# Kernel tuning notes

Hardware: AMD Instinct MI355X
Metric: run time of the kernel (lower is better)

## Reference

```python
import jax, jax.numpy as jnp
import numpy as np

EPS = 1e-3  # Keras BatchNormalization default epsilon
HEADS = 4
KEY_DEPTH = 16   # k
INTRA = 1        # u
VAL_DEPTH = 64   # v = kernel_out // heads = 256 // 4
C_IN = 256
B, HH, WW = 16, 32, 32
N = HH * WW      # == size of positional embedding


def setup_inputs() -> dict:
    key = jax.random.key(0)
    ks = jax.random.split(key, 6)
    x = jax.random.normal(ks[0], (B, HH, WW, C_IN), dtype=jnp.float32)
    # 1x1 conv kernels == dense matrices over the channel dim
    Wq = jax.random.normal(ks[1], (C_IN, KEY_DEPTH * HEADS), dtype=jnp.float32) * 0.05
    Wk = jax.random.normal(ks[2], (C_IN, KEY_DEPTH * INTRA), dtype=jnp.float32) * 0.05
    Wv = jax.random.normal(ks[3], (C_IN, VAL_DEPTH * INTRA), dtype=jnp.float32) * 0.05
    # BatchNorm (inference mode) parameters
    gamma_q = jnp.ones((KEY_DEPTH * HEADS,), jnp.float32)
    beta_q = jnp.zeros((KEY_DEPTH * HEADS,), jnp.float32)
    mean_q = jnp.zeros((KEY_DEPTH * HEADS,), jnp.float32)
    var_q = jnp.ones((KEY_DEPTH * HEADS,), jnp.float32)
    gamma_v = jnp.ones((VAL_DEPTH * INTRA,), jnp.float32)
    beta_v = jnp.zeros((VAL_DEPTH * INTRA,), jnp.float32)
    mean_v = jnp.zeros((VAL_DEPTH * INTRA,), jnp.float32)
    var_v = jnp.ones((VAL_DEPTH * INTRA,), jnp.float32)
    # Positional embedding: [size, size, key_depth, intra_depth], uniform init
    E = jax.random.uniform(ks[4], (N, N, KEY_DEPTH, INTRA), dtype=jnp.float32)
    return {
        'x': x, 'Wq': Wq, 'Wk': Wk, 'Wv': Wv,
        'gamma_q': gamma_q, 'beta_q': beta_q, 'mean_q': mean_q, 'var_q': var_q,
        'gamma_v': gamma_v, 'beta_v': beta_v, 'mean_v': mean_v, 'var_v': var_v,
        'E': E,
    }


def _bn(t, gamma, beta, mean, var):
    return gamma * (t - mean) / jnp.sqrt(var + EPS) + beta


def reference(x, Wq, Wk, Wv, gamma_q, beta_q, mean_q, var_q,
              gamma_v, beta_v, mean_v, var_v, E):
    b, hh, ww, _ = x.shape
    n = hh * ww
    # 1x1 conv projections (context c == x)
    q = jnp.einsum('bhwc,cd->bhwd', x, Wq)           # [b,hh,ww,h*k]
    k = jnp.einsum('bhwc,cd->bhwd', x, Wk)           # [b,hh,ww,u*k]
    v = jnp.einsum('bhwc,cd->bhwd', x, Wv)           # [b,hh,ww,u*v]
    q = _bn(q, gamma_q, beta_q, mean_q, var_q)
    v = _bn(v, gamma_v, beta_v, mean_v, var_v)
    # softmax over the channel axis (faithful to the source code)
    k = jax.nn.softmax(k, axis=-1)
    # rearranges: b hh ww (h k) -> b h k n ; b hh ww (u k) -> b u k n ; b hh ww (u v) -> b u v n
    q = q.reshape(b, n, HEADS, KEY_DEPTH).transpose(0, 2, 3, 1)   # [b,h,k,n]
    k = k.reshape(b, n, INTRA, KEY_DEPTH).transpose(0, 2, 3, 1)   # [b,u,k,n]
    v = v.reshape(b, n, INTRA, VAL_DEPTH).transpose(0, 2, 3, 1)   # [b,u,v,n]
    # content lambda: sum over intra-depth and positions
    lam_c = jnp.einsum('bukn,buvn->bkv', k, v)                    # [b,k,v]
    Yc = jnp.einsum('bhkn,bkv->bhvn', q, lam_c)                   # [b,h,v,n]
    # positional lambdas: E[n,m,k,u] contracted with v[b,u,v,m]
    lam_p = jnp.einsum('nmku,buvm->bnkv', E, v)                   # [b,n,k,v]
    Yp = jnp.einsum('bhkn,bnkv->bhvn', q, lam_p)                  # [b,h,v,n]
    Y = Yc + Yp                                                    # [b,h,v,n]
    # b h v n -> b hh ww (h v)
    out = Y.transpose(0, 3, 1, 2).reshape(b, hh, ww, HEADS * VAL_DEPTH)
    return out
```

## Files before the change

### kernel.cpp

```cpp
#include <hip/hip_runtime.h>
#include <stdint.h>

#define EPS 1e-3f

typedef __bf16 bf16x8 __attribute__((ext_vector_type(8)));
typedef float  f32x4  __attribute__((ext_vector_type(4)));

static __device__ __forceinline__ uint16_t f2bf(float f) {
  union { float f; uint32_t u; } v; v.f = f;
  uint32_t u = v.u;
  uint32_t r = u + 0x7fffu + ((u >> 16) & 1u);
  return (uint16_t)(r >> 16);
}
static __device__ __forceinline__ uint32_t pack2bf(float lo, float hi) {
  union { uint16_t h[2]; uint32_t u; } r;
  r.h[0] = f2bf(lo); r.h[1] = f2bf(hi);
  return r.u;
}
static __device__ __forceinline__ void gload_lds16(const void* g, void* l) {
  __builtin_amdgcn_global_load_lds(
      (const __attribute__((address_space(1))) unsigned int*)g,
      (__attribute__((address_space(3))) unsigned int*)l, 16, 0, 0);
}

__global__ __launch_bounds__(256) void wprep(
    const float* __restrict__ Wq, const float* __restrict__ Wk,
    const float* __restrict__ Wv, uint16_t* __restrict__ WtP)
{
  const int col = blockIdx.x, t = threadIdx.x;
  float val = (col < 64) ? Wq[t * 64 + col]
            : (col < 80) ? Wk[t * 16 + (col - 64)]
                         : Wv[t * 64 + (col - 80)];
  WtP[col * 264 + t] = f2bf(val);
}

__global__ __launch_bounds__(256) void proj_mfma(
    const float* __restrict__ x, const uint16_t* __restrict__ WtP,
    const float* __restrict__ gq, const float* __restrict__ bq,
    const float* __restrict__ mq, const float* __restrict__ vq,
    const float* __restrict__ gv, const float* __restrict__ bv,
    const float* __restrict__ mv, const float* __restrict__ vvp,
    float* __restrict__ Qf, uint16_t* __restrict__ VbfT,
    float* __restrict__ part)
{
  __shared__ __align__(16) char smem[111616];
  uint16_t* const xA = (uint16_t*)smem;
  char* const Wt = smem + 33792;

  const int t = threadIdx.x;
  const int wid = t >> 6, lane = t & 63;
  const int bid = blockIdx.x;
  const int b = bid >> 4, mc = bid & 15;
  const int r0 = b * 1024 + mc * 64;

#pragma unroll
  for (int i = 0; i < 19; ++i) {
    int off = (i * 256 + t) * 16;
    gload_lds16((const char*)WtP + off, Wt + off);
  }
  {
    const int row = t >> 2, ks0 = (t & 3) * 64;
    const float* src = x + (size_t)(r0 + row) * 256 + ks0;
    uint16_t* dstp = xA + row * 264 + ks0;
#pragma unroll
    for (int i = 0; i < 8; ++i) {
      float4 d0 = *(const float4*)(src + i * 8);
      float4 d1 = *(const float4*)(src + i * 8 + 4);
      union { uint16_t u[8]; uint4 q; } pk;
      pk.u[0] = f2bf(d0.x); pk.u[1] = f2bf(d0.y);
      pk.u[2] = f2bf(d0.z); pk.u[3] = f2bf(d0.w);
      pk.u[4] = f2bf(d1.x); pk.u[5] = f2bf(d1.y);
      pk.u[6] = f2bf(d1.z); pk.u[7] = f2bf(d1.w);
      *(uint4*)(dstp + i * 8) = pk.q;
    }
  }
  __syncthreads();

  f32x4 acc[9];
#pragma unroll
  for (int f = 0; f < 9; ++f) acc[f] = f32x4{0.f, 0.f, 0.f, 0.f};
  const int arow = wid * 16 + (lane & 15);
#pragma unroll
  for (int kst = 0; kst < 8; ++kst) {
    const int sb = kst * 64 + ((lane >> 4) << 4);
    bf16x8 af = *(const bf16x8*)((const char*)xA + arow * 528 + sb);
#pragma unroll
    for (int f = 0; f < 9; ++f) {
      const int crow = f * 16 + (lane & 15);
      bf16x8 bfr = *(const bf16x8*)(Wt + crow * 528 + sb);
      acc[f] = __builtin_amdgcn_mfma_f32_16x16x32_bf16(af, bfr, acc[f], 0, 0, 0);
    }
  }

  const int cl = lane & 15;
  const int rbase = wid * 16 + ((lane >> 4) << 2);

  float qs[4], qb[4], qm[4], vs[4], vb[4], vm[4];
#pragma unroll
  for (int f = 0; f < 4; ++f) {
    const int c = f * 16 + cl;
    qs[f] = gq[c] * rsqrtf(vq[c] + EPS); qb[f] = bq[c]; qm[f] = mq[c];
    vs[f] = gv[c] * rsqrtf(vvp[c] + EPS); vb[f] = bv[c]; vm[f] = mv[c];
  }
#pragma unroll
  for (int f = 0; f < 4; ++f)
#pragma unroll
    for (int r = 0; r < 4; ++r)
      Qf[(size_t)(r0 + rbase + r) * 64 + f * 16 + cl] =
          (acc[f][r] - qm[f]) * qs[f] + qb[f];
  float ex[4];
#pragma unroll
  for (int r = 0; r < 4; ++r) {
    float kv = acc[4][r];
    float mx = kv;
#pragma unroll
    for (int d = 1; d < 16; d <<= 1) mx = fmaxf(mx, __shfl_xor(mx, d, 64));
    float e = __expf(kv - mx);
    float sm = e;
#pragma unroll
    for (int d = 1; d < 16; d <<= 1) sm += __shfl_xor(sm, d, 64);
    ex[r] = e / sm;
  }
  float vv[4][4];
#pragma unroll
  for (int f = 0; f < 4; ++f)
#pragma unroll
    for (int r = 0; r < 4; ++r)
      vv[f][r] = (acc[5 + f][r] - vm[f]) * vs[f] + vb[f];

  __syncthreads();
  float* const vt = (float*)smem;
  float* const ks = (float*)(smem + 64 * 65 * 4);
#pragma unroll
  for (int r = 0; r < 4; ++r) ks[(rbase + r) * 20 + cl] = ex[r];
#pragma unroll
  for (int f = 0; f < 4; ++f)
#pragma unroll
    for (int r = 0; r < 4; ++r) vt[(rbase + r) * 65 + f * 16 + cl] = vv[f][r];
  __syncthreads();

  {
    const int v = t & 63, grp = t >> 6;
#pragma unroll
    for (int h = 0; h < 2; ++h) {
      union { uint16_t u16[8]; uint4 q; } pk;
#pragma unroll
      for (int i = 0; i < 8; ++i)
        pk.u16[i] = f2bf(vt[(grp * 16 + h * 8 + i) * 65 + v]);
      *(uint4*)&VbfT[(size_t)(b * 64 + v) * 1024 + mc * 64 + grp * 16 + h * 8] = pk.q;
    }
  }
  {
    const int kq = t >> 6, v = t & 63;
    float a0 = 0.f, a1 = 0.f, a2 = 0.f, a3 = 0.f;
#pragma unroll 4
    for (int m = 0; m < 64; ++m) {
      float vvx = vt[m * 65 + v];
      a0 = fmaf(ks[m * 20 + kq * 4 + 0], vvx, a0);
      a1 = fmaf(ks[m * 20 + kq * 4 + 1], vvx, a1);
      a2 = fmaf(ks[m * 20 + kq * 4 + 2], vvx, a2);
      a3 = fmaf(ks[m * 20 + kq * 4 + 3], vvx, a3);
    }
    float* dst = part + ((size_t)(b * 16 + mc) << 10) + (kq * 4) * 64 + v;
    dst[0] = a0; dst[64] = a1; dst[128] = a2; dst[192] = a3;
  }
}

__global__ __launch_bounds__(256) void lamc_reduce(const float* __restrict__ part,
                                                   float* __restrict__ Lc)
{
  const int gid = blockIdx.x * 256 + threadIdx.x;
  const int b = gid >> 10, r = gid & 1023;
  const float* p = part + ((size_t)b << 14) + r;
  float s = 0.f;
#pragma unroll
  for (int mc = 0; mc < 16; ++mc) s += p[mc << 10];
  Lc[((size_t)b << 10) + r] = s;
}

__global__ __launch_bounds__(512, 2) void gemm_out(
    const float* __restrict__ E,
    const uint16_t* __restrict__ VbfT,
    const float* __restrict__ Qf,
    const float* __restrict__ Lc,
    float* __restrict__ out)
{
  __shared__ __align__(16) char smem[131072];
  char* const A0 = smem;
  char* const B0 = smem + 32768;
  char* const A1 = smem + 65536;
  char* const B1 = smem + 98304;

  const int t = threadIdx.x;
  const int wid = t >> 6, lane = t & 63;
  const int wm = wid >> 2, wn = wid & 3;
  const int bid = blockIdx.x;
  const int xcd = bid & 7, idx = bid >> 3;
  const int rb = xcd * 8 + (idx >> 2);
  const int cb = idx & 3;
  const int col0 = cb * 256;
  const int n0 = rb * 16;

  const int kq = t & 3;
  const int mp = (t >> 2) & 31;
  const int nb = t >> 7;
  const float* Eb = E + ((size_t)n0 << 14);

  int awoff[4][4];
#pragma unroll
  for (int it = 0; it < 4; ++it)
#pragma unroll
    for (int j = 0; j < 4; ++j) {
      int row = (it * 4 + nb) * 16 + kq * 4 + j;
      awoff[it][j] = row * 128 + ((mp * 4) ^ ((row & 7) << 4));
    }

  const uint16_t* bptr[4];
  int bdst[4];
  {
    const uint16_t* Bb = VbfT + ((size_t)col0 << 10);
#pragma unroll
    for (int it = 0; it < 4; ++it) {
      int id = it * 512 + t;
      int row = id >> 3, seg = id & 7;
      bptr[it] = Bb + (row << 10) + ((seg ^ (row & 7)) << 3);
      bdst[it] = id * 16;
    }
  }

  f32x4 acc[8][4];
#pragma unroll
  for (int i = 0; i < 8; ++i)
#pragma unroll
    for (int j = 0; j < 4; ++j) acc[i][j] = f32x4{0.f, 0.f, 0.f, 0.f};

  float4 ra[4], rbx[4];

#pragma unroll
  for (int it = 0; it < 4; ++it) {
    size_t base = ((size_t)(it * 4 + nb) << 14) + ((size_t)(mp * 2) << 4) + (kq << 2);
    ra[it]  = *(const float4*)(Eb + base);
    rbx[it] = *(const float4*)(Eb + base + 16);
  }
#pragma unroll
  for (int it = 0; it < 4; ++it) gload_lds16(bptr[it], B0 + bdst[it]);
#pragma unroll
  for (int it = 0; it < 4; ++it) {
    const float* da = (const float*)&ra[it];
    const float* db = (const float*)&rbx[it];
#pragma unroll
    for (int j = 0; j < 4; ++j)
      *(uint32_t*)(A0 + awoff[it][j]) = pack2bf(da[j], db[j]);
  }
  __syncthreads();

#pragma unroll 1
  for (int kt = 0; kt < 16; ++kt) {
    char* Ac = (kt & 1) ? A1 : A0;
    char* Bc = (kt & 1) ? B1 : B0;
    char* An = (kt & 1) ? A0 : A1;
    char* Bn = (kt & 1) ? B0 : B1;
    if (kt < 15) {
      const int m0n = (kt + 1) * 64;
#pragma unroll
      for (int it = 0; it < 4; ++it) {
        size_t base = ((size_t)(it * 4 + nb) << 14) +
                      ((size_t)(m0n + mp * 2) << 4) + (kq << 2);
        ra[it]  = *(const float4*)(Eb + base);
        rbx[it] = *(const float4*)(Eb + base + 16);
      }
#pragma unroll
      for (int it = 0; it < 4; ++it) gload_lds16(bptr[it] + m0n, Bn + bdst[it]);
    }
    __builtin_amdgcn_s_setprio(1);
#pragma unroll
    for (int kk = 0; kk < 2; ++kk) {
      bf16x8 a[8], b[4];
      const int s = kk * 4 + (lane >> 4);
#pragma unroll
      for (int i = 0; i < 8; ++i) {
        int row = wm * 128 + i * 16 + (lane & 15);
        a[i] = *(const bf16x8*)(Ac + row * 128 + ((s ^ (row & 7)) << 4));
      }
#pragma unroll
      for (int j = 0; j < 4; ++j) {
        int row = wn * 64 + j * 16 + (lane & 15);
        b[j] = *(const bf16x8*)(Bc + row * 128 + ((s ^ (row & 7)) << 4));
      }
#pragma unroll
      for (int i = 0; i < 8; ++i)
#pragma unroll
        for (int j = 0; j < 4; ++j)
          acc[i][j] = __builtin_amdgcn_mfma_f32_16x16x32_bf16(a[i], b[j], acc[i][j], 0, 0, 0);
    }
    __builtin_amdgcn_s_setprio(0);
    if (kt < 15) {
#pragma unroll
      for (int it = 0; it < 4; ++it) {
        const float* da = (const float*)&ra[it];
        const float* db = (const float*)&rbx[it];
#pragma unroll
        for (int j = 0; j < 4; ++j)
          *(uint32_t*)(An + awoff[it][j]) = pack2bf(da[j], db[j]);
      }
    }
    __syncthreads();
  }

  float* Cs = (float*)smem;
  const int b0 = cb * 4;
#pragma unroll
  for (int p = 0; p < 4; ++p) {
    if (wm == (p >> 1)) {
#pragma unroll
      for (int il = 0; il < 4; ++il) {
        const int i = ((p & 1) << 2) + il;
#pragma unroll
        for (int j = 0; j < 4; ++j) {
          const int col = wn * 64 + j * 16 + (lane & 15);
          const int bb = b0 + (col >> 6), v = col & 63;
#pragma unroll
          for (int r = 0; r < 4; ++r) {
            const int rl = il * 16 + ((lane >> 4) << 2) + r;
            const int k = rl & 15;
            Cs[rl * 258 + col] = acc[i][j][r] + Lc[(size_t)(((bb << 4) + k) << 6) + v];
          }
        }
      }
    }
    __syncthreads();
    {
      const int v = t & 63;
#pragma unroll
      for (int c = 0; c < 8; ++c) {
        const int combo = (wid << 3) + c;
        const int n_l = combo >> 4;
        const int b_l = (combo >> 2) & 3;
        const int h = combo & 3;
        const int n = n0 + (p << 2) + n_l;
        const int bb = b0 + b_l;
        const float* qp = Qf + (((size_t)(bb << 10) + n) << 6) + (h << 4);
        float sum = 0.f;
#pragma unroll
        for (int k = 0; k < 16; ++k)
          sum = fmaf(qp[k], Cs[((n_l << 4) + k) * 258 + (b_l << 6) + v], sum);
        out[(((size_t)(bb << 10) + n) << 8) + (h << 6) + v] = sum;
      }
    }
    __syncthreads();
  }
}

extern "C" void kernel_launch(void* const* d_in, const int* in_sizes, int n_in,
                              void* d_out, int out_size, void* d_ws, size_t ws_size,
                              hipStream_t stream) {
  const float* x   = (const float*)d_in[0];
  const float* Wq  = (const float*)d_in[1];
  const float* Wk  = (const float*)d_in[2];
  const float* Wv  = (const float*)d_in[3];
  const float* gq  = (const float*)d_in[4];
  const float* bq  = (const float*)d_in[5];
  const float* mq  = (const float*)d_in[6];
  const float* vq  = (const float*)d_in[7];
  const float* gv  = (const float*)d_in[8];
  const float* bv  = (const float*)d_in[9];
  const float* mv  = (const float*)d_in[10];
  const float* vvp = (const float*)d_in[11];
  const float* E   = (const float*)d_in[12];
  float* out = (float*)d_out;

  char* ws = (char*)d_ws;
  uint16_t* VbfT = (uint16_t*)(ws);
  float*    Qf   = (float*)(ws + (size_t)(2 << 20));
  float*    part = (float*)(ws + (size_t)(6 << 20));
  float*    Lc   = (float*)(ws + (size_t)(7 << 20));
  uint16_t* WtP  = (uint16_t*)(ws + (size_t)(7 << 20) + 65536);

  hipLaunchKernelGGL(wprep, dim3(144), dim3(256), 0, stream, Wq, Wk, Wv, WtP);
  hipLaunchKernelGGL(proj_mfma, dim3(256), dim3(256), 0, stream, x, WtP,
                     gq, bq, mq, vq, gv, bv, mv, vvp, Qf, VbfT, part);
  hipLaunchKernelGGL(lamc_reduce, dim3(64), dim3(256), 0, stream, part, Lc);
  hipLaunchKernelGGL(gemm_out, dim3(256), dim3(512), 0, stream, E, VbfT, Qf, Lc, out);
}
```

Baseline: 75.38 us.

## Double proj_mfma block size to 128 rows and use native bf16 conversion

The projection kernel now runs 128 blocks of 512 threads, each handling 128 rows instead of 64, so the weight tile loaded into LDS is amortised over twice as many rows. The partial lambda_c reduction is split into two halves per block so the part buffer layout stays the same. Manual round-to-nearest-even bf16 packing is replaced with the compiler's native __bf16 conversion, which may map to hardware convert instructions. The risks are fewer blocks than CUs and a larger LDS footprint (about 140 KB) per block.

```diff
diff --git a/kernel.cpp b/kernel.cpp
--- a/kernel.cpp
+++ b/kernel.cpp
@@ -7,14 +7,11 @@
 typedef float  f32x4  __attribute__((ext_vector_type(4)));
 
 static __device__ __forceinline__ uint16_t f2bf(float f) {
-  union { float f; uint32_t u; } v; v.f = f;
-  uint32_t u = v.u;
-  uint32_t r = u + 0x7fffu + ((u >> 16) & 1u);
-  return (uint16_t)(r >> 16);
-}
-static __device__ __forceinline__ uint32_t pack2bf(float lo, float hi) {
-  union { uint16_t h[2]; uint32_t u; } r;
-  r.h[0] = f2bf(lo); r.h[1] = f2bf(hi);
+  union { __bf16 b; uint16_t u; } r; r.b = (__bf16)f; return r.u;
+}
+static __device__ __forceinline__ uint32_t cvt2(float lo, float hi) {
+  union { __bf16 b[2]; uint32_t u; } r;
+  r.b[0] = (__bf16)lo; r.b[1] = (__bf16)hi;
   return r.u;
 }
 static __device__ __forceinline__ void gload_lds16(const void* g, void* l) {
@@ -34,7 +31,7 @@
   WtP[col * 264 + t] = f2bf(val);
 }
 
-__global__ __launch_bounds__(256) void proj_mfma(
+__global__ __launch_bounds__(512) void proj_mfma(
     const float* __restrict__ x, const uint16_t* __restrict__ WtP,
     const float* __restrict__ gq, const float* __restrict__ bq,
     const float* __restrict__ mq, const float* __restrict__ vq,
@@ -43,19 +40,19 @@
     float* __restrict__ Qf, uint16_t* __restrict__ VbfT,
     float* __restrict__ part)
 {
-  __shared__ __align__(16) char smem[111616];
+  __shared__ __align__(16) char smem[143616];
   uint16_t* const xA = (uint16_t*)smem;
-  char* const Wt = smem + 33792;
+  char* const Wt = smem + 67584;
 
   const int t = threadIdx.x;
   const int wid = t >> 6, lane = t & 63;
   const int bid = blockIdx.x;
-  const int b = bid >> 4, mc = bid & 15;
-  const int r0 = b * 1024 + mc * 64;
-
-#pragma unroll
-  for (int i = 0; i < 19; ++i) {
-    int off = (i * 256 + t) * 16;
+  const int b = bid >> 3, mc = bid & 7;
+  const int r0 = b * 1024 + mc * 128;
+
+#pragma unroll
+  for (int i = 0; i < 10; ++i) {
+    int off = (i * 512 + t) * 16;
     gload_lds16((const char*)WtP + off, Wt + off);
   }
   {
@@ -66,12 +63,10 @@
     for (int i = 0; i < 8; ++i) {
       float4 d0 = *(const float4*)(src + i * 8);
       float4 d1 = *(const float4*)(src + i * 8 + 4);
-      union { uint16_t u[8]; uint4 q; } pk;
-      pk.u[0] = f2bf(d0.x); pk.u[1] = f2bf(d0.y);
-      pk.u[2] = f2bf(d0.z); pk.u[3] = f2bf(d0.w);
-      pk.u[4] = f2bf(d1.x); pk.u[5] = f2bf(d1.y);
-      pk.u[6] = f2bf(d1.z); pk.u[7] = f2bf(d1.w);
-      *(uint4*)(dstp + i * 8) = pk.q;
+      uint4 q;
+      q.x = cvt2(d0.x, d0.y); q.y = cvt2(d0.z, d0.w);
+      q.z = cvt2(d1.x, d1.y); q.w = cvt2(d1.z, d1.w);
+      *(uint4*)(dstp + i * 8) = q;
     }
   }
   __syncthreads();
@@ -130,7 +125,7 @@
 
   __syncthreads();
   float* const vt = (float*)smem;
-  float* const ks = (float*)(smem + 64 * 65 * 4);
+  float* const ks = (float*)(smem + 128 * 65 * 4);
 #pragma unroll
   for (int r = 0; r < 4; ++r) ks[(rbase + r) * 20 + cl] = ex[r];
 #pragma unroll
@@ -143,25 +138,27 @@
     const int v = t & 63, grp = t >> 6;
 #pragma unroll
     for (int h = 0; h < 2; ++h) {
-      union { uint16_t u16[8]; uint4 q; } pk;
-#pragma unroll
-      for (int i = 0; i < 8; ++i)
-        pk.u16[i] = f2bf(vt[(grp * 16 + h * 8 + i) * 65 + v]);
-      *(uint4*)&VbfT[(size_t)(b * 64 + v) * 1024 + mc * 64 + grp * 16 + h * 8] = pk.q;
+      uint4 q;
+      q.x = cvt2(vt[(grp * 16 + h * 8 + 0) * 65 + v], vt[(grp * 16 + h * 8 + 1) * 65 + v]);
+      q.y = cvt2(vt[(grp * 16 + h * 8 + 2) * 65 + v], vt[(grp * 16 + h * 8 + 3) * 65 + v]);
+      q.z = cvt2(vt[(grp * 16 + h * 8 + 4) * 65 + v], vt[(grp * 16 + h * 8 + 5) * 65 + v]);
+      q.w = cvt2(vt[(grp * 16 + h * 8 + 6) * 65 + v], vt[(grp * 16 + h * 8 + 7) * 65 + v]);
+      *(uint4*)&VbfT[(size_t)(b * 64 + v) * 1024 + mc * 128 + grp * 16 + h * 8] = q;
     }
   }
   {
-    const int kq = t >> 6, v = t & 63;
+    const int kq = (t >> 6) & 3, half = t >> 8, v = t & 63;
+    const int mbase = half * 64;
     float a0 = 0.f, a1 = 0.f, a2 = 0.f, a3 = 0.f;
 #pragma unroll 4
     for (int m = 0; m < 64; ++m) {
-      float vvx = vt[m * 65 + v];
-      a0 = fmaf(ks[m * 20 + kq * 4 + 0], vvx, a0);
-      a1 = fmaf(ks[m * 20 + kq * 4 + 1], vvx, a1);
-      a2 = fmaf(ks[m * 20 + kq * 4 + 2], vvx, a2);
-      a3 = fmaf(ks[m * 20 + kq * 4 + 3], vvx, a3);
-    }
-    float* dst = part + ((size_t)(b * 16 + mc) << 10) + (kq * 4) * 64 + v;
+      float vvx = vt[(mbase + m) * 65 + v];
+      a0 = fmaf(ks[(mbase + m) * 20 + kq * 4 + 0], vvx, a0);
+      a1 = fmaf(ks[(mbase + m) * 20 + kq * 4 + 1], vvx, a1);
+      a2 = fmaf(ks[(mbase + m) * 20 + kq * 4 + 2], vvx, a2);
+      a3 = fmaf(ks[(mbase + m) * 20 + kq * 4 + 3], vvx, a3);
+    }
+    float* dst = part + ((size_t)(b * 16 + mc * 2 + half) << 10) + (kq * 4) * 64 + v;
     dst[0] = a0; dst[64] = a1; dst[128] = a2; dst[192] = a3;
   }
 }
@@ -250,7 +247,7 @@
     const float* db = (const float*)&rbx[it];
 #pragma unroll
     for (int j = 0; j < 4; ++j)
-      *(uint32_t*)(A0 + awoff[it][j]) = pack2bf(da[j], db[j]);
+      *(uint32_t*)(A0 + awoff[it][j]) = cvt2(da[j], db[j]);
   }
   __syncthreads();
 
@@ -301,7 +298,7 @@
         const float* db = (const float*)&rbx[it];
 #pragma unroll
         for (int j = 0; j < 4; ++j)
-          *(uint32_t*)(An + awoff[it][j]) = pack2bf(da[j], db[j]);
+          *(uint32_t*)(An + awoff[it][j]) = cvt2(da[j], db[j]);
       }
     }
     __syncthreads();
@@ -377,7 +374,7 @@
   uint16_t* WtP  = (uint16_t*)(ws + (size_t)(7 << 20) + 65536);
 
   hipLaunchKernelGGL(wprep, dim3(144), dim3(256), 0, stream, Wq, Wk, Wv, WtP);
-  hipLaunchKernelGGL(proj_mfma, dim3(256), dim3(256), 0, stream, x, WtP,
+  hipLaunchKernelGGL(proj_mfma, dim3(128), dim3(512), 0, stream, x, WtP,
                      gq, bq, mq, vq, gv, bv, mv, vvp, Qf, VbfT, part);
   hipLaunchKernelGGL(lamc_reduce, dim3(64), dim3(256), 0, stream, part, Lc);
   hipLaunchKernelGGL(gemm_out, dim3(256), dim3(512), 0, stream, E, VbfT, Qf, Lc, out);
```

After: 77.58 us. +2.9%, slower.
